# Kernel optimization log

Hardware: AMD Instinct MI355X
Metric: run time of the kernel (lower is better)

The kernel has to match this reference:

```python
import jax, jax.numpy as jnp
import numpy as np

MARGIN = 1.0
EPS = 1e-12  # safe sqrt/normalize clamp; used entries have magnitude >> EPS


def _normalize(x):
    return x / jnp.maximum(jnp.linalg.norm(x, axis=-1, keepdims=True), EPS)


def _cdist(x, y):
    # Pairwise L2 distances, matches torch.cdist(p=2)
    sq = (jnp.sum(x * x, axis=-1)[:, None]
          + jnp.sum(y * y, axis=-1)[None, :]
          - 2.0 * (x @ y.T))
    return jnp.sqrt(jnp.maximum(sq, EPS))


def setup_inputs() -> dict:
    key = jax.random.key(0)
    k1, k2, k3 = jax.random.split(key, 3)
    B, P, D = 4096, 2, 256
    anchor = jax.random.normal(k1, (B, D), dtype=jnp.float32)
    positive = jax.random.normal(k2, (B, P, D), dtype=jnp.float32)
    labels = jax.random.randint(k3, (B,), 0, 200)
    return {"anchor": anchor, "positive": positive, "labels": labels}


def reference(anchor, positive, labels):
    a = _normalize(anchor)            # [B, D]
    p = _normalize(positive)          # [B, P, D]
    B = a.shape[0]
    all_labels = jnp.concatenate([labels, labels])           # [2B]
    neg_mask = all_labels[None, :] != labels[:, None]        # [B, 2B]
    idx = jnp.arange(B)
    losses = []
    for v in range(p.shape[1]):  # loop over small fixed num_positives
        feats = jnp.concatenate([a, p[:, v]], axis=0)        # [2B, D]
        dist = _cdist(feats, feats)                          # [2B, 2B]
        pos_dist = dist[idx, idx + B]                        # [B]
        # hard negative mining: min distance over different-label columns
        neg_dist = jnp.min(jnp.where(neg_mask, dist[:B], jnp.inf), axis=1)  # [B]
        losses.append(jnp.maximum(pos_dist - neg_dist + MARGIN, 0.0))
    return jnp.mean(jnp.stack(losses))
```

## Files before the change

kernel.cpp:

```cpp
#include <hip/hip_runtime.h>
#include <hip/hip_bf16.h>

#define NB    4096
#define ND    256
#define NP    2
#define TOT   (NB * 3)
#define NCHUNK 48
#define COLS_PER_CHUNK 256
#define TILES 16
#define IMIN_SENT (-1073741824)
#define INV_SCALE (1.0f / 16129.0f)

typedef float f32x4 __attribute__((ext_vector_type(4)));
typedef int   i32x4 __attribute__((ext_vector_type(4)));

#define WS_F_OFF    0
#define WS_POS_OFF  (TOT * 256)
#define WS_NEG_OFF  (WS_POS_OFF + NB * NP * 4)

__global__ void norm_pos_kernel(const float* __restrict__ anchor,
                                const float* __restrict__ positive,
                                unsigned char* __restrict__ F2,
                                float* __restrict__ posArr,
                                int* __restrict__ negmax) {
    if (blockIdx.x < 48) negmax[blockIdx.x * 256 + threadIdx.x] = IMIN_SENT;

    int wid = threadIdx.x >> 6, lane = threadIdx.x & 63;
    int row = blockIdx.x * 4 + wid;
    int group = row >> 4, r15 = row & 15;
    int kk = lane >> 4, quad = (lane >> 2) & 3, jj = (lane & 3) * 4;
    int* dst = (int*)(F2 + (size_t)group * 4096 + kk * 1024 + (quad * 16 + r15) * 16 + jj);

    if (row < NB) {
        const float* src = anchor + (size_t)row * ND;
        float4 x = *(const float4*)(src + lane * 4);
        float ss = x.x * x.x + x.y * x.y + x.z * x.z + x.w * x.w;
        #pragma unroll
        for (int m = 1; m < 64; m <<= 1) ss += __shfl_xor(ss, m, 64);
        float inv = 127.0f / fmaxf(sqrtf(ss), 1e-12f);
        int b0 = (int)rintf(x.x * inv) & 0xff;
        int b1 = (int)rintf(x.y * inv) & 0xff;
        int b2 = (int)rintf(x.z * inv) & 0xff;
        int b3 = (int)rintf(x.w * inv) & 0xff;
        *dst = b0 | (b1 << 8) | (b2 << 16) | (b3 << 24);
    } else {
        int q = row - NB;
        int v = q >> 12;
        int j = q & (NB - 1);
        const float* sp = positive + (size_t)(j * NP + v) * ND;
        const float* sa = anchor + (size_t)j * ND;
        float4 xp = *(const float4*)(sp + lane * 4);
        float4 xa = *(const float4*)(sa + lane * 4);
        float sspv = xp.x * xp.x + xp.y * xp.y + xp.z * xp.z + xp.w * xp.w;
        float ssa  = xa.x * xa.x + xa.y * xa.y + xa.z * xa.z + xa.w * xa.w;
        float dot  = xa.x * xp.x + xa.y * xp.y + xa.z * xp.z + xa.w * xp.w;
        #pragma unroll
        for (int m = 1; m < 64; m <<= 1) {
            sspv += __shfl_xor(sspv, m, 64);
            ssa  += __shfl_xor(ssa, m, 64);
            dot  += __shfl_xor(dot, m, 64);
        }
        float invp = 127.0f / fmaxf(sqrtf(sspv), 1e-12f);
        int b0 = (int)rintf(xp.x * invp) & 0xff;
        int b1 = (int)rintf(xp.y * invp) & 0xff;
        int b2 = (int)rintf(xp.z * invp) & 0xff;
        int b3 = (int)rintf(xp.w * invp) & 0xff;
        *dst = b0 | (b1 << 8) | (b2 << 16) | (b3 << 24);
        if (lane == 0) {
            float inva = 1.0f / fmaxf(sqrtf(ssa), 1e-12f);
            float invpf = invp * (1.0f / 127.0f);
            float dn = dot * inva * invpf;
            float sq = 2.0f - 2.0f * dn;
            posArr[j * NP + v] = sqrtf(fmaxf(sq, 1e-12f));
        }
    }
}

__global__ __launch_bounds__(512) void gram_max_kernel(
        const unsigned char* __restrict__ F2,
        const int* __restrict__ labels,
        int* __restrict__ negmax) {
    __shared__ unsigned char ldsB[TILES * 4096];
    __shared__ int slab[COLS_PER_CHUNK];
    int tid = threadIdx.x;
    int wid = tid >> 6, lane = tid & 63;
    int l15 = lane & 15, quad = lane >> 4;

    int id = blockIdx.x;
    int chunk = id >> 4;
    int rbi   = id & 15;

    int rowBase = rbi * 256 + wid * 32;
    int col0 = chunk * COLS_PER_CHUNK;
    int part = chunk >> 4;

    i32x4 af[2][4];
    #pragma unroll
    for (int s = 0; s < 2; ++s) {
        const unsigned char* ab = F2 + (size_t)(rbi * 16 + wid * 2 + s) * 4096 + lane * 16;
        #pragma unroll
        for (int kk = 0; kk < 4; ++kk)
            af[s][kk] = *(const i32x4*)(ab + kk * 1024);
    }
    unsigned rlp[2];
    #pragma unroll
    for (int s = 0; s < 2; ++s) {
        const int* lb = labels + rowBase + s * 16 + quad * 4;
        rlp[s] = (unsigned)lb[0] | ((unsigned)lb[1] << 8)
               | ((unsigned)lb[2] << 16) | ((unsigned)lb[3] << 24);
    }
    if (tid < COLS_PER_CHUNK) slab[tid] = labels[(col0 & (NB - 1)) + tid];

    {
        const float4* src = (const float4*)(F2 + (size_t)chunk * 16 * 4096);
        float4* dst = (float4*)ldsB;
        #pragma unroll
        for (int j = 0; j < 8; ++j)
            dst[tid + j * 512] = src[tid + j * 512];
    }

    int vmax[2][4];
    #pragma unroll
    for (int s = 0; s < 2; ++s)
        #pragma unroll
        for (int r = 0; r < 4; ++r) vmax[s][r] = IMIN_SENT;

    __syncthreads();

    #pragma unroll 2
    for (int ct = 0; ct < TILES; ++ct) {
        i32x4 bfr[4];
        #pragma unroll
        for (int kk = 0; kk < 4; ++kk)
            bfr[kk] = *(const i32x4*)&ldsB[ct * 4096 + kk * 1024 + lane * 16];

        int lc = slab[ct * 16 + l15];
        unsigned lcq = (unsigned)lc * 0x01010101u;

        i32x4 acc[2];
        #pragma unroll
        for (int s = 0; s < 2; ++s) acc[s] = (i32x4){0, 0, 0, 0};
        #pragma unroll
        for (int kk = 0; kk < 4; ++kk)
            #pragma unroll
            for (int s = 0; s < 2; ++s)
                acc[s] = __builtin_amdgcn_mfma_i32_16x16x64_i8(af[s][kk], bfr[kk], acc[s], 0, 0, 0);

        #pragma unroll
        for (int s = 0; s < 2; ++s) {
            unsigned x = rlp[s] ^ lcq;
            #pragma unroll
            for (int r = 0; r < 4; ++r) {
                bool neq = ((x >> (8 * r)) & 0xffu) != 0u;
                int cand = neq ? acc[s][r] : IMIN_SENT;
                vmax[s][r] = vmax[s][r] > cand ? vmax[s][r] : cand;
            }
        }
    }

    #pragma unroll
    for (int m = 1; m < 16; m <<= 1)
        #pragma unroll
        for (int s = 0; s < 2; ++s)
            #pragma unroll
            for (int r = 0; r < 4; ++r) {
                int o = __shfl_xor(vmax[s][r], m, 64);
                vmax[s][r] = vmax[s][r] > o ? vmax[s][r] : o;
            }

    if (l15 == 0) {
        #pragma unroll
        for (int s = 0; s < 2; ++s)
            #pragma unroll
            for (int r = 0; r < 4; ++r) {
                int row = rowBase + s * 16 + quad * 4 + r;
                atomicMax(&negmax[part * NB + row], vmax[s][r]);
            }
    }
}

__global__ void finalize_kernel(const int* __restrict__ negmax,
                                const float* __restrict__ posArr,
                                float* __restrict__ out) {
    int row = blockIdx.x * 256 + threadIdx.x;
    int ia = negmax[row];
    int i0 = negmax[NB + row];
    int i1 = negmax[2 * NB + row];
    int m0 = ia > i0 ? ia : i0;
    int m1 = ia > i1 ? ia : i1;
    float d0 = (float)m0 * INV_SCALE;
    float d1 = (float)m1 * INV_SCALE;
    float n0 = sqrtf(fmaxf(2.0f - 2.0f * d0, 1e-12f));
    float n1 = sqrtf(fmaxf(2.0f - 2.0f * d1, 1e-12f));
    float l = fmaxf(posArr[row * 2 + 0] - n0 + 1.0f, 0.0f)
            + fmaxf(posArr[row * 2 + 1] - n1 + 1.0f, 0.0f);
    int lane = threadIdx.x & 63, wid = threadIdx.x >> 6;
    #pragma unroll
    for (int m = 1; m < 64; m <<= 1) l += __shfl_xor(l, m, 64);
    __shared__ float wsum[4];
    if (lane == 0) wsum[wid] = l;
    __syncthreads();
    if (threadIdx.x == 0) {
        float s = wsum[0] + wsum[1] + wsum[2] + wsum[3];
        atomicAdd(out, s * (1.0f / (NB * NP)));
    }
}

extern "C" void kernel_launch(void* const* d_in, const int* in_sizes, int n_in,
                              void* d_out, int out_size, void* d_ws, size_t ws_size,
                              hipStream_t stream) {
    const float* anchor   = (const float*)d_in[0];
    const float* positive = (const float*)d_in[1];
    const int*   labels   = (const int*)d_in[2];
    float* out = (float*)d_out;

    unsigned char* F2 = (unsigned char*)((char*)d_ws + WS_F_OFF);
    float* posArr     = (float*)((char*)d_ws + WS_POS_OFF);
    int*   negmax     = (int*)((char*)d_ws + WS_NEG_OFF);

    hipMemsetAsync(d_out, 0, sizeof(float), stream);
    norm_pos_kernel<<<TOT / 4, 256, 0, stream>>>(anchor, positive, F2, posArr, negmax);
    gram_max_kernel<<<(NB / 256) * NCHUNK, 512, 0, stream>>>(F2, labels, negmax);
    finalize_kernel<<<NB / 256, 256, 0, stream>>>(negmax, posArr, out);
}
```

Measured before the change: 86.47 us.

## Fuse finalize into gram kernel via last-block reduction and use async LDS loads

```diff
diff --git a/kernel.cpp b/kernel.cpp
--- a/kernel.cpp
+++ b/kernel.cpp
@@ -17,13 +17,20 @@
 #define WS_F_OFF    0
 #define WS_POS_OFF  (TOT * 256)
 #define WS_NEG_OFF  (WS_POS_OFF + NB * NP * 4)
+#define WS_CNT_OFF  (WS_NEG_OFF + 3 * NB * 4)
+
+__device__ __forceinline__ int agent_load(const int* p) {
+    return __hip_atomic_load(p, __ATOMIC_RELAXED, __HIP_MEMORY_SCOPE_AGENT);
+}
 
 __global__ void norm_pos_kernel(const float* __restrict__ anchor,
                                 const float* __restrict__ positive,
                                 unsigned char* __restrict__ F2,
                                 float* __restrict__ posArr,
-                                int* __restrict__ negmax) {
+                                int* __restrict__ negmax,
+                                int* __restrict__ cnt) {
     if (blockIdx.x < 48) negmax[blockIdx.x * 256 + threadIdx.x] = IMIN_SENT;
+    if (blockIdx.x == 48 && threadIdx.x == 0) cnt[0] = 0;
 
     int wid = threadIdx.x >> 6, lane = threadIdx.x & 63;
     int row = blockIdx.x * 4 + wid;
@@ -76,12 +83,18 @@
     }
 }
 
-__global__ __launch_bounds__(512) void gram_max_kernel(
+__global__ __launch_bounds__(256) void gram_max_kernel(
         const unsigned char* __restrict__ F2,
         const int* __restrict__ labels,
-        int* __restrict__ negmax) {
+        const float* __restrict__ posArr,
+        int* __restrict__ negmax,
+        int* __restrict__ cnt,
+        float* __restrict__ out) {
     __shared__ unsigned char ldsB[TILES * 4096];
     __shared__ int slab[COLS_PER_CHUNK];
+    __shared__ int lastFlag;
+    __shared__ float wsum[4];
+
     int tid = threadIdx.x;
     int wid = tid >> 6, lane = tid & 63;
     int l15 = lane & 15, quad = lane >> 4;
@@ -90,38 +103,39 @@
     int chunk = id >> 4;
     int rbi   = id & 15;
 
-    int rowBase = rbi * 256 + wid * 32;
+    int rowBase = rbi * 256 + wid * 64;
     int col0 = chunk * COLS_PER_CHUNK;
     int part = chunk >> 4;
 
-    i32x4 af[2][4];
-    #pragma unroll
-    for (int s = 0; s < 2; ++s) {
-        const unsigned char* ab = F2 + (size_t)(rbi * 16 + wid * 2 + s) * 4096 + lane * 16;
+    {
+        const unsigned char* src = F2 + (size_t)chunk * 65536 + wid * 16384 + lane * 16;
+        unsigned char* dst = ldsB + wid * 16384;
+        #pragma unroll
+        for (int j = 0; j < 16; ++j)
+            __builtin_amdgcn_global_load_lds((const unsigned int*)(src + j * 1024),
+                                             (unsigned int*)(dst + j * 1024), 16, 0, 0);
+    }
+
+    i32x4 af[4][4];
+    #pragma unroll
+    for (int s = 0; s < 4; ++s) {
+        const unsigned char* ab = F2 + (size_t)(rbi * 16 + wid * 4 + s) * 4096 + lane * 16;
         #pragma unroll
         for (int kk = 0; kk < 4; ++kk)
             af[s][kk] = *(const i32x4*)(ab + kk * 1024);
     }
-    unsigned rlp[2];
-    #pragma unroll
-    for (int s = 0; s < 2; ++s) {
+    unsigned rlp[4];
+    #pragma unroll
+    for (int s = 0; s < 4; ++s) {
         const int* lb = labels + rowBase + s * 16 + quad * 4;
         rlp[s] = (unsigned)lb[0] | ((unsigned)lb[1] << 8)
                | ((unsigned)lb[2] << 16) | ((unsigned)lb[3] << 24);
     }
-    if (tid < COLS_PER_CHUNK) slab[tid] = labels[(col0 & (NB - 1)) + tid];
-
-    {
-        const float4* src = (const float4*)(F2 + (size_t)chunk * 16 * 4096);
-        float4* dst = (float4*)ldsB;
-        #pragma unroll
-        for (int j = 0; j < 8; ++j)
-            dst[tid + j * 512] = src[tid + j * 512];
-    }
-
-    int vmax[2][4];
-    #pragma unroll
-    for (int s = 0; s < 2; ++s)
+    slab[tid] = labels[(col0 & (NB - 1)) + tid];
+
+    int vmax[4][4];
+    #pragma unroll
+    for (int s = 0; s < 4; ++s)
         #pragma unroll
         for (int r = 0; r < 4; ++r) vmax[s][r] = IMIN_SENT;
 
@@ -129,25 +143,26 @@
 
     #pragma unroll 2
     for (int ct = 0; ct < TILES; ++ct) {
+        const unsigned char* bbase = ldsB + ct * 4096 + lane * 16;
         i32x4 bfr[4];
         #pragma unroll
         for (int kk = 0; kk < 4; ++kk)
-            bfr[kk] = *(const i32x4*)&ldsB[ct * 4096 + kk * 1024 + lane * 16];
+            bfr[kk] = *(const i32x4*)(bbase + kk * 1024);
 
         int lc = slab[ct * 16 + l15];
         unsigned lcq = (unsigned)lc * 0x01010101u;
 
-        i32x4 acc[2];
-        #pragma unroll
-        for (int s = 0; s < 2; ++s) acc[s] = (i32x4){0, 0, 0, 0};
+        i32x4 acc[4];
+        #pragma unroll
+        for (int s = 0; s < 4; ++s) acc[s] = (i32x4){0, 0, 0, 0};
         #pragma unroll
         for (int kk = 0; kk < 4; ++kk)
             #pragma unroll
-            for (int s = 0; s < 2; ++s)
+            for (int s = 0; s < 4; ++s)
                 acc[s] = __builtin_amdgcn_mfma_i32_16x16x64_i8(af[s][kk], bfr[kk], acc[s], 0, 0, 0);
 
         #pragma unroll
-        for (int s = 0; s < 2; ++s) {
+        for (int s = 0; s < 4; ++s) {
             unsigned x = rlp[s] ^ lcq;
             #pragma unroll
             for (int r = 0; r < 4; ++r) {
@@ -161,7 +176,7 @@
     #pragma unroll
     for (int m = 1; m < 16; m <<= 1)
         #pragma unroll
-        for (int s = 0; s < 2; ++s)
+        for (int s = 0; s < 4; ++s)
             #pragma unroll
             for (int r = 0; r < 4; ++r) {
                 int o = __shfl_xor(vmax[s][r], m, 64);
@@ -170,40 +185,44 @@
 
     if (l15 == 0) {
         #pragma unroll
-        for (int s = 0; s < 2; ++s)
+        for (int s = 0; s < 4; ++s)
             #pragma unroll
             for (int r = 0; r < 4; ++r) {
                 int row = rowBase + s * 16 + quad * 4 + r;
                 atomicMax(&negmax[part * NB + row], vmax[s][r]);
             }
     }
-}
-
-__global__ void finalize_kernel(const int* __restrict__ negmax,
-                                const float* __restrict__ posArr,
-                                float* __restrict__ out) {
-    int row = blockIdx.x * 256 + threadIdx.x;
-    int ia = negmax[row];
-    int i0 = negmax[NB + row];
-    int i1 = negmax[2 * NB + row];
-    int m0 = ia > i0 ? ia : i0;
-    int m1 = ia > i1 ? ia : i1;
-    float d0 = (float)m0 * INV_SCALE;
-    float d1 = (float)m1 * INV_SCALE;
-    float n0 = sqrtf(fmaxf(2.0f - 2.0f * d0, 1e-12f));
-    float n1 = sqrtf(fmaxf(2.0f - 2.0f * d1, 1e-12f));
-    float l = fmaxf(posArr[row * 2 + 0] - n0 + 1.0f, 0.0f)
-            + fmaxf(posArr[row * 2 + 1] - n1 + 1.0f, 0.0f);
-    int lane = threadIdx.x & 63, wid = threadIdx.x >> 6;
-    #pragma unroll
-    for (int m = 1; m < 64; m <<= 1) l += __shfl_xor(l, m, 64);
-    __shared__ float wsum[4];
-    if (lane == 0) wsum[wid] = l;
+
+    __threadfence();
+    if (tid == 0) {
+        int old = atomicAdd(cnt, 1);
+        lastFlag = (old == (int)gridDim.x - 1);
+    }
     __syncthreads();
-    if (threadIdx.x == 0) {
-        float s = wsum[0] + wsum[1] + wsum[2] + wsum[3];
-        atomicAdd(out, s * (1.0f / (NB * NP)));
-    }
+    if (!lastFlag) return;
+
+    float lsum = 0.0f;
+    #pragma unroll 4
+    for (int k = 0; k < 16; ++k) {
+        int row = tid + k * 256;
+        int ia = agent_load(&negmax[row]);
+        int i0 = agent_load(&negmax[NB + row]);
+        int i1 = agent_load(&negmax[2 * NB + row]);
+        int m0 = ia > i0 ? ia : i0;
+        int m1 = ia > i1 ? ia : i1;
+        float d0 = (float)m0 * INV_SCALE;
+        float d1 = (float)m1 * INV_SCALE;
+        float n0 = sqrtf(fmaxf(2.0f - 2.0f * d0, 1e-12f));
+        float n1 = sqrtf(fmaxf(2.0f - 2.0f * d1, 1e-12f));
+        float2 pr = *(const float2*)&posArr[row * 2];
+        lsum += fmaxf(pr.x - n0 + 1.0f, 0.0f) + fmaxf(pr.y - n1 + 1.0f, 0.0f);
+    }
+    #pragma unroll
+    for (int m = 1; m < 64; m <<= 1) lsum += __shfl_xor(lsum, m, 64);
+    if (lane == 0) wsum[wid] = lsum;
+    __syncthreads();
+    if (tid == 0)
+        out[0] = (wsum[0] + wsum[1] + wsum[2] + wsum[3]) * (1.0f / (NB * NP));
 }
 
 extern "C" void kernel_launch(void* const* d_in, const int* in_sizes, int n_in,
@@ -217,9 +236,8 @@
     unsigned char* F2 = (unsigned char*)((char*)d_ws + WS_F_OFF);
     float* posArr     = (float*)((char*)d_ws + WS_POS_OFF);
     int*   negmax     = (int*)((char*)d_ws + WS_NEG_OFF);
-
-    hipMemsetAsync(d_out, 0, sizeof(float), stream);
-    norm_pos_kernel<<<TOT / 4, 256, 0, stream>>>(anchor, positive, F2, posArr, negmax);
-    gram_max_kernel<<<(NB / 256) * NCHUNK, 512, 0, stream>>>(F2, labels, negmax);
-    finalize_kernel<<<NB / 256, 256, 0, stream>>>(negmax, posArr, out);
-}
+    int*   cnt        = (int*)((char*)d_ws + WS_CNT_OFF);
+
+    norm_pos_kernel<<<TOT / 4, 256, 0, stream>>>(anchor, positive, F2, posArr, negmax, cnt);
+    gram_max_kernel<<<(NB / 256) * NCHUNK, 256, 0, stream>>>(F2, labels, posArr, negmax, cnt, out);
+}
```

After: 131.1 us. +51.6%, slower.
